# Performance work log

Hardware: AMD Instinct MI355X
Metric: run time of the kernel (lower is better)

## Reference

```python
import jax, jax.numpy as jnp
import numpy as np

N_NEURONS = 50000   # dense_shape[0]
N_INPUT = 17400     # dense_shape[1] (LGN units)
NNZ = 1_000_000     # number of sparse synapses
B, T = 1, 256       # batch, timesteps
BKG_SPIKE_RATE = 4  # hardcoded in original call()


def setup_inputs() -> dict:
    key = jax.random.key(0)
    k1, k2, k3, k4, k5 = jax.random.split(key, 5)
    rows = jax.random.randint(k1, (NNZ,), 0, N_NEURONS, dtype=jnp.int32)
    cols = jax.random.randint(k2, (NNZ,), 0, N_INPUT, dtype=jnp.int32)
    weights = jax.random.normal(k3, (NNZ,), dtype=jnp.float32)
    bkg_weights = jax.random.normal(k4, (N_NEURONS,), dtype=jnp.float32)
    inp = jax.random.uniform(k5, (B, T, N_INPUT), dtype=jnp.float32)
    return {"inp": inp, "weights": weights, "bkg_weights": bkg_weights,
            "rows": rows, "cols": cols}


def reference(inp, weights, bkg_weights, rows, cols):
    b, t, n_in = inp.shape
    x = inp.reshape(b * t, n_in)                     # (BT, n_input)
    # Sparse COO matmul: current[n, bt] = sum_{k: rows[k]==n} weights[k] * x[bt, cols[k]]
    # Equivalent to tf.sparse.sparse_dense_matmul(W_sparse, x, adjoint_b=True).
    contrib = weights[:, None] * x.T[cols]           # (nnz, BT)
    cur = jax.ops.segment_sum(contrib, rows, num_segments=N_NEURONS)  # (N, BT)
    cur = cur.T                                      # (BT, N) -- tf.transpose
    # Background noise: uniform(0,1) < 1 is always True, so rest == BKG_SPIKE_RATE.
    u = jax.random.uniform(jax.random.key(42), (b, t, BKG_SPIKE_RATE))
    rest = jnp.sum((u < 1.0).astype(inp.dtype), axis=-1)   # (b, t), constant 4
    noise = bkg_weights[None, None, :] * rest[..., None]   # (b, t, N)
    return cur.reshape(b, t, -1) + noise
```

## Files before the change

### kernel.cpp

```cpp
#include <hip/hip_runtime.h>

#define N_NEURONS 50000
#define N_INPUT   17400
#define NNZ_TOTAL 1000000
#define T_STEPS   256
#define ELL_CAP   64

typedef float f4_t __attribute__((ext_vector_type(4)));

__global__ __launch_bounds__(256) void transpose_kernel(
    const float* __restrict__ inp, ushort* __restrict__ xTb) {
    __shared__ float tile[32][33];
    const int bx = blockIdx.x;
    const int by = blockIdx.y;
    const int tx = threadIdx.x;
    const int ty = threadIdx.y;

    const int c = bx * 32 + tx;
#pragma unroll
    for (int i = 0; i < 4; ++i) {
        const int r = by * 32 + ty + i * 8;
        if (c < N_INPUT)
            tile[ty + i * 8][tx] = inp[r * N_INPUT + c];
    }
    __syncthreads();

    const int t = by * 32 + tx;
#pragma unroll
    for (int i = 0; i < 4; ++i) {
        const int rr = bx * 32 + ty + i * 8;
        if (rr < N_INPUT) {
            unsigned u = __float_as_uint(tile[tx][ty + i * 8]);
            u += 0x7fffu + ((u >> 16) & 1u);
            xTb[(size_t)rr * T_STEPS + t] = (ushort)(u >> 16);
        }
    }
}

__global__ __launch_bounds__(256) void ell_build_kernel(
    const int* __restrict__ rows, const int* __restrict__ cols,
    const float* __restrict__ w, int* __restrict__ cnt,
    unsigned* __restrict__ ell) {
    const int i = blockIdx.x * blockDim.x + threadIdx.x;
    if (i < NNZ_TOTAL) {
        const int r = rows[i];
        const int p = atomicAdd(&cnt[r], 1);
        if (p < ELL_CAP) {
            unsigned u = __float_as_uint(w[i]);
            u += 0x7fffu + ((u >> 16) & 1u);
            ell[(size_t)r * ELL_CAP + p] =
                ((unsigned)cols[i] << 16) | (u >> 16);
        }
    }
}

__global__ __launch_bounds__(256) void spmm_kernel(
    const uint2* __restrict__ xT2,
    const int* __restrict__ cnt, const unsigned* __restrict__ ell,
    const float* __restrict__ bkg, float* __restrict__ out) {
    __shared__ float lds[16][260];
    const int tid  = threadIdx.x;
    const int lane = tid & 63;
    const int wv   = tid >> 6;
    const int base = blockIdx.x * 16;
    const int n0   = base + wv * 4;

    const int4   cv  = *(const int4*)&cnt[n0];
    const float4 bgv = *(const float4*)&bkg[n0];
    unsigned ev[4];
#pragma unroll
    for (int q = 0; q < 4; ++q)
        ev[q] = ell[(size_t)(n0 + q) * ELL_CAP + lane];

#pragma unroll
    for (int q = 0; q < 4; ++q) {
        const int c = min((q == 0) ? cv.x : (q == 1) ? cv.y
                          : (q == 2) ? cv.z : cv.w, ELL_CAP);
        const int cpad = (c + 7) & ~7;
        float4 acc = make_float4(0.f, 0.f, 0.f, 0.f);

        for (int k0 = 0; k0 < cpad; k0 += 8) {
            unsigned e[8];
            uint2 xv[8];
#pragma unroll
            for (int j = 0; j < 8; ++j) e[j] = __shfl(ev[q], k0 + j);
#pragma unroll
            for (int j = 0; j < 8; ++j)
                xv[j] = xT2[(size_t)(e[j] >> 16) * 64 + lane];
#pragma unroll
            for (int j = 0; j < 8; ++j) {
                const float wk = __uint_as_float(e[j] << 16);
                acc.x = fmaf(wk, __uint_as_float((xv[j].x & 0xffffu) << 16), acc.x);
                acc.y = fmaf(wk, __uint_as_float(xv[j].x & 0xffff0000u),     acc.y);
                acc.z = fmaf(wk, __uint_as_float((xv[j].y & 0xffffu) << 16), acc.z);
                acc.w = fmaf(wk, __uint_as_float(xv[j].y & 0xffff0000u),     acc.w);
            }
        }
        const float b4 = 4.0f * ((q == 0) ? bgv.x : (q == 1) ? bgv.y
                                 : (q == 2) ? bgv.z : bgv.w);
        acc.x += b4; acc.y += b4; acc.z += b4; acc.w += b4;
        *(float4*)&lds[wv * 4 + q][lane * 4] = acc;
    }
    __syncthreads();

    const int c4 = (tid & 3) * 4;
    const int t0 = tid >> 2;
#pragma unroll
    for (int t = t0; t < T_STEPS; t += 64) {
        f4_t v;
        v.x = lds[c4 + 0][t];
        v.y = lds[c4 + 1][t];
        v.z = lds[c4 + 2][t];
        v.w = lds[c4 + 3][t];
        __builtin_nontemporal_store(
            v, (f4_t*)&out[(size_t)t * N_NEURONS + base + c4]);
    }
}

extern "C" void kernel_launch(void* const* d_in, const int* in_sizes, int n_in,
                              void* d_out, int out_size, void* d_ws,
                              size_t ws_size, hipStream_t stream) {
    const float* inp     = (const float*)d_in[0];
    const float* weights = (const float*)d_in[1];
    const float* bkg     = (const float*)d_in[2];
    const int*   rows    = (const int*)d_in[3];
    const int*   cols    = (const int*)d_in[4];
    float*       out     = (float*)d_out;

    size_t off = 0;
    auto wsalloc = [&](size_t bytes) -> void* {
        void* p = (char*)d_ws + off;
        off += (bytes + 255) & ~size_t(255);
        return p;
    };
    ushort*   xTb = (ushort*)wsalloc(sizeof(ushort) * N_INPUT * T_STEPS);
    int*      cnt = (int*)wsalloc(sizeof(int) * N_NEURONS);
    unsigned* ell = (unsigned*)wsalloc(sizeof(unsigned) * N_NEURONS * ELL_CAP);
    (void)ws_size;

    const size_t zlen = ((char*)ell + sizeof(unsigned) * N_NEURONS * ELL_CAP)
                        - (char*)cnt;
    (void)hipMemsetAsync(cnt, 0, zlen, stream);

    transpose_kernel<<<dim3((N_INPUT + 31) / 32, T_STEPS / 32), dim3(32, 8), 0,
                       stream>>>(inp, xTb);

    const int nb = (NNZ_TOTAL + 255) / 256;
    ell_build_kernel<<<nb, 256, 0, stream>>>(rows, cols, weights, cnt, ell);

    spmm_kernel<<<N_NEURONS / 16, 256, 0, stream>>>(
        (const uint2*)xTb, cnt, ell, bkg, out);
}
```

Before: 201.4 us.

## Skip ELL memset and partition ELL build by row groups for locality

The memset now clears only the counts and no longer the full 12.8 MB ELL buffer. The SpMM kernel masks slots past each row's count to zero, so stale entries read as column 0 with weight 0. The ELL build launches 1024 blocks. Each handles one of 8 row groups and scans a chunk of the nonzeros, processing only rows in its group, so atomic and scatter traffic should stay within a smaller address range that may map to one XCD's L2. In exchange every nonzero's row index is read 8 times.

```diff
diff --git a/kernel.cpp b/kernel.cpp
--- a/kernel.cpp
+++ b/kernel.cpp
@@ -5,6 +5,9 @@
 #define NNZ_TOTAL 1000000
 #define T_STEPS   256
 #define ELL_CAP   64
+#define GROUPS    8
+#define ROWS_PER_GROUP 6250
+#define BLKS_PER_GROUP 128
 
 typedef float f4_t __attribute__((ext_vector_type(4)));
 
@@ -41,15 +44,24 @@
     const int* __restrict__ rows, const int* __restrict__ cols,
     const float* __restrict__ w, int* __restrict__ cnt,
     unsigned* __restrict__ ell) {
-    const int i = blockIdx.x * blockDim.x + threadIdx.x;
-    if (i < NNZ_TOTAL) {
+    const int g    = blockIdx.x & (GROUPS - 1);
+    const int blk  = blockIdx.x >> 3;
+    const int r_lo = g * ROWS_PER_GROUP;
+    const int r_hi = r_lo + ROWS_PER_GROUP;
+    const int per_blk = (NNZ_TOTAL + BLKS_PER_GROUP - 1) / BLKS_PER_GROUP;
+    const int i_lo = blk * per_blk;
+    const int i_hi = min(i_lo + per_blk, NNZ_TOTAL);
+
+    for (int i = i_lo + (int)threadIdx.x; i < i_hi; i += 256) {
         const int r = rows[i];
-        const int p = atomicAdd(&cnt[r], 1);
-        if (p < ELL_CAP) {
-            unsigned u = __float_as_uint(w[i]);
-            u += 0x7fffu + ((u >> 16) & 1u);
-            ell[(size_t)r * ELL_CAP + p] =
-                ((unsigned)cols[i] << 16) | (u >> 16);
+        if (r >= r_lo && r < r_hi) {
+            const int p = atomicAdd(&cnt[r], 1);
+            if (p < ELL_CAP) {
+                unsigned u = __float_as_uint(w[i]);
+                u += 0x7fffu + ((u >> 16) & 1u);
+                ell[(size_t)r * ELL_CAP + p] =
+                    ((unsigned)cols[i] << 16) | (u >> 16);
+            }
         }
     }
 }
@@ -67,16 +79,18 @@
 
     const int4   cv  = *(const int4*)&cnt[n0];
     const float4 bgv = *(const float4*)&bkg[n0];
+    const int cs[4] = {min(cv.x, ELL_CAP), min(cv.y, ELL_CAP),
+                       min(cv.z, ELL_CAP), min(cv.w, ELL_CAP)};
     unsigned ev[4];
 #pragma unroll
-    for (int q = 0; q < 4; ++q)
-        ev[q] = ell[(size_t)(n0 + q) * ELL_CAP + lane];
+    for (int q = 0; q < 4; ++q) {
+        const unsigned raw = ell[(size_t)(n0 + q) * ELL_CAP + lane];
+        ev[q] = (lane < cs[q]) ? raw : 0u;
+    }
 
 #pragma unroll
     for (int q = 0; q < 4; ++q) {
-        const int c = min((q == 0) ? cv.x : (q == 1) ? cv.y
-                          : (q == 2) ? cv.z : cv.w, ELL_CAP);
-        const int cpad = (c + 7) & ~7;
+        const int cpad = (cs[q] + 7) & ~7;
         float4 acc = make_float4(0.f, 0.f, 0.f, 0.f);
 
         for (int k0 = 0; k0 < cpad; k0 += 8) {
@@ -138,15 +152,13 @@
     unsigned* ell = (unsigned*)wsalloc(sizeof(unsigned) * N_NEURONS * ELL_CAP);
     (void)ws_size;
 
-    const size_t zlen = ((char*)ell + sizeof(unsigned) * N_NEURONS * ELL_CAP)
-                        - (char*)cnt;
-    (void)hipMemsetAsync(cnt, 0, zlen, stream);
+    (void)hipMemsetAsync(cnt, 0, sizeof(int) * N_NEURONS, stream);
 
     transpose_kernel<<<dim3((N_INPUT + 31) / 32, T_STEPS / 32), dim3(32, 8), 0,
                        stream>>>(inp, xTb);
 
-    const int nb = (NNZ_TOTAL + 255) / 256;
-    ell_build_kernel<<<nb, 256, 0, stream>>>(rows, cols, weights, cnt, ell);
+    ell_build_kernel<<<GROUPS * BLKS_PER_GROUP, 256, 0, stream>>>(
+        rows, cols, weights, cnt, ell);
 
     spmm_kernel<<<N_NEURONS / 16, 256, 0, stream>>>(
         (const uint2*)xTb, cnt, ell, bkg, out);
```

Result: slower. 206.3 us (+2.4%).
